# Kernel optimization log

Hardware: AMD Instinct MI355X
Metric: run time of the kernel (lower is better)

The kernel has to match this reference:

```python
import jax, jax.numpy as jnp
import numpy as np

N = 1536
IN_CH = 256
HEADS = 8
OUT_CH = 8
HC = HEADS * OUT_CH  # 64
NEG_SLOPE = 0.2
MASK_BIAS = -1e9


def setup_inputs() -> dict:
    key = jax.random.key(0)
    k1, k2, k3, k4, k5 = jax.random.split(key, 5)
    nodes_ft = jax.random.normal(k1, (N, IN_CH), dtype=jnp.float32)
    u = jax.random.uniform(k2, (N, N), dtype=jnp.float32)
    adj = (u < 0.05) | (jnp.arange(N)[:, None] == jnp.arange(N)[None, :])
    adj_bias_mat = jnp.where(adj, 0.0, MASK_BIAS).astype(jnp.float32)
    weight = jax.random.normal(k3, (IN_CH, HC), dtype=jnp.float32) * (2.0 / (IN_CH + HC)) ** 0.5
    conv_weight1 = jax.random.normal(k4, (HC, HC), dtype=jnp.float32) * (1.0 / HC) ** 0.5
    conv_weight2 = jax.random.normal(k5, (HC, HC), dtype=jnp.float32) * (1.0 / HC) ** 0.5
    return {
        "nodes_ft": nodes_ft,
        "adj_bias_mat": adj_bias_mat,
        "weight": weight,
        "conv_weight1": conv_weight1,
        "conv_weight2": conv_weight2,
    }


def reference(nodes_ft, adj_bias_mat, weight, conv_weight1, conv_weight2):
    # node_hidden_state: [n, HC]
    nhs = nodes_ft @ weight
    f1 = nhs @ conv_weight1  # [n, HC]
    f2 = nhs @ conv_weight2  # [n, HC]
    # dense pairwise additive logits: [n, n, HC]
    logits = f1[:, None, :] + f2[None, :, :]
    scores = jax.nn.leaky_relu(logits, negative_slope=NEG_SLOPE) + adj_bias_mat[:, :, None]
    coefs = jax.nn.softmax(scores, axis=1)  # normalize over source-node dim
    # vals[i, c] = sum_j coefs[i, j, c] * nhs[i, c]  (eval mode: no dropout)
    vals = jnp.sum(coefs * nhs[:, None, :], axis=1)
    return vals
```

## Files before the change

### kernel.cpp

```cpp
#include <hip/hip_runtime.h>


#define N_NODES 1536
#define IN_CH 256
#define HC 64

__global__ __launch_bounds__(128) void nhs_gemm(const float* __restrict__ A,
                                                const float* __restrict__ W,
                                                float* __restrict__ out) {
    const int cq  = threadIdx.x & 15;
    const int row = (blockIdx.x << 3) + (threadIdx.x >> 4);

    const float* a = A + row * IN_CH;
    const float* w = W + (cq << 2);

    float4 acc = make_float4(0.f, 0.f, 0.f, 0.f);
#pragma unroll 4
    for (int k = 0; k < IN_CH; k += 4) {
        const float4 av = *(const float4*)(a + k);
        const float4 w0 = *(const float4*)(w + (k + 0) * HC);
        const float4 w1 = *(const float4*)(w + (k + 1) * HC);
        const float4 w2 = *(const float4*)(w + (k + 2) * HC);
        const float4 w3 = *(const float4*)(w + (k + 3) * HC);
        acc.x = fmaf(av.w, w3.x, fmaf(av.z, w2.x, fmaf(av.y, w1.x, fmaf(av.x, w0.x, acc.x))));
        acc.y = fmaf(av.w, w3.y, fmaf(av.z, w2.y, fmaf(av.y, w1.y, fmaf(av.x, w0.y, acc.y))));
        acc.z = fmaf(av.w, w3.z, fmaf(av.z, w2.z, fmaf(av.y, w1.z, fmaf(av.x, w0.z, acc.z))));
        acc.w = fmaf(av.w, w3.w, fmaf(av.z, w2.w, fmaf(av.y, w1.w, fmaf(av.x, w0.w, acc.w))));
    }
    *(float4*)(out + row * HC + (cq << 2)) = acc;
}

extern "C" void kernel_launch(void* const* d_in, const int* in_sizes, int n_in,
                              void* d_out, int out_size, void* d_ws, size_t ws_size,
                              hipStream_t stream) {
    const float* nodes_ft = (const float*)d_in[0];
    const float* weight   = (const float*)d_in[2];
    float* out = (float*)d_out;

    nhs_gemm<<<N_NODES / 8, 128, 0, stream>>>(nodes_ft, weight, out);
}
```

Before: 73.36 us.

## Split the K dimension across warps with a shared-memory reduction in the node GEMM

Each block now handles 4 rows, and the 256-wide reduction is split into 8 chunks, each computed by its own group of threads. Partial float4 sums are combined through shared memory after a barrier. This gives 384 blocks of 512 threads and shorter per-thread dependency chains, to fill more CUs and hide load latency on a small GEMM. The cost is an extra shared-memory pass, a `__syncthreads`, and a final reduction done by only 64 threads.

```diff
diff --git a/kernel.cpp b/kernel.cpp
--- a/kernel.cpp
+++ b/kernel.cpp
@@ -4,19 +4,25 @@
 #define N_NODES 1536
 #define IN_CH 256
 #define HC 64
+#define KS 8
+#define ROWS 4
+#define KCHUNK (IN_CH / KS)
+#define BLOCK (ROWS * 16 * KS)
 
-__global__ __launch_bounds__(128) void nhs_gemm(const float* __restrict__ A,
-                                                const float* __restrict__ W,
-                                                float* __restrict__ out) {
-    const int cq  = threadIdx.x & 15;
-    const int row = (blockIdx.x << 3) + (threadIdx.x >> 4);
+__global__ __launch_bounds__(BLOCK, 4) void nhs_gemm(const float* __restrict__ A,
+                                                     const float* __restrict__ W,
+                                                     float* __restrict__ out) {
+    const int cq = threadIdx.x & 15;
+    const int r  = (threadIdx.x >> 4) & (ROWS - 1);
+    const int ks = threadIdx.x >> 6;
+    const int row = blockIdx.x * ROWS + r;
 
-    const float* a = A + row * IN_CH;
-    const float* w = W + (cq << 2);
+    const float* a = A + row * IN_CH + ks * KCHUNK;
+    const float* w = W + (cq << 2) + ks * KCHUNK * HC;
 
     float4 acc = make_float4(0.f, 0.f, 0.f, 0.f);
-#pragma unroll 4
-    for (int k = 0; k < IN_CH; k += 4) {
+#pragma unroll
+    for (int k = 0; k < KCHUNK; k += 4) {
         const float4 av = *(const float4*)(a + k);
         const float4 w0 = *(const float4*)(w + (k + 0) * HC);
         const float4 w1 = *(const float4*)(w + (k + 1) * HC);
@@ -27,7 +33,22 @@
         acc.z = fmaf(av.w, w3.z, fmaf(av.z, w2.z, fmaf(av.y, w1.z, fmaf(av.x, w0.z, acc.z))));
         acc.w = fmaf(av.w, w3.w, fmaf(av.z, w2.w, fmaf(av.y, w1.w, fmaf(av.x, w0.w, acc.w))));
     }
-    *(float4*)(out + row * HC + (cq << 2)) = acc;
+
+    __shared__ float4 red[KS][ROWS * 16];
+    red[ks][(r << 4) | cq] = acc;
+    __syncthreads();
+
+    if (threadIdx.x < ROWS * 16) {
+        float4 s = red[0][threadIdx.x];
+#pragma unroll
+        for (int i = 1; i < KS; ++i) {
+            const float4 t = red[i][threadIdx.x];
+            s.x += t.x; s.y += t.y; s.z += t.z; s.w += t.w;
+        }
+        const int rr = threadIdx.x >> 4;
+        const int cc = threadIdx.x & 15;
+        *(float4*)(out + (blockIdx.x * ROWS + rr) * HC + (cc << 2)) = s;
+    }
 }
 
 extern "C" void kernel_launch(void* const* d_in, const int* in_sizes, int n_in,
@@ -37,5 +58,5 @@
     const float* weight   = (const float*)d_in[2];
     float* out = (float*)d_out;
 
-    nhs_gemm<<<N_NODES / 8, 128, 0, stream>>>(nodes_ft, weight, out);
+    nhs_gemm<<<N_NODES / ROWS, BLOCK, 0, stream>>>(nodes_ft, weight, out);
 }
```

Measured after the change: 69.67 us. 1.05x faster.
